# Performance work log

Measured on AMD Instinct MI355X. Metric: run time of the kernel, lower is better.

The kernel has to match this reference:

```python
import jax, jax.numpy as jnp
import numpy as np

B, S, H, L = 64, 512, 768, 9


def setup_inputs() -> dict:
    key = jax.random.key(0)
    ks = jax.random.split(key, 9)
    hidden_states = jax.random.normal(ks[0], (B, S, H), dtype=jnp.float32)
    classifier_w = jax.random.normal(ks[1], (H, L), dtype=jnp.float32) * 0.02
    classifier_b = jax.random.normal(ks[2], (L,), dtype=jnp.float32) * 0.02
    class_weights = jax.random.uniform(ks[3], (L,), dtype=jnp.float32, minval=0.5, maxval=2.0)
    start_transitions = jax.random.normal(ks[4], (L,), dtype=jnp.float32) * 0.1
    end_transitions = jax.random.normal(ks[5], (L,), dtype=jnp.float32) * 0.1
    transitions = jax.random.normal(ks[6], (L, L), dtype=jnp.float32) * 0.1
    labels = jax.random.randint(ks[7], (B, S), 0, L, dtype=jnp.int64)
    special = jax.random.uniform(ks[8], (B, S)) < 0.1
    labels = jnp.where(special, jnp.asarray(-100, labels.dtype), labels)
    # variable-length sequences: attention_mask = 1 for t < length
    lengths = jax.random.randint(jax.random.fold_in(key, 7), (B,), S // 2, S + 1)
    attention_mask = (jnp.arange(S)[None, :] < lengths[:, None]).astype(jnp.int64)
    return dict(hidden_states=hidden_states, classifier_w=classifier_w,
                classifier_b=classifier_b, class_weights=class_weights,
                start_transitions=start_transitions, end_transitions=end_transitions,
                transitions=transitions, labels=labels, attention_mask=attention_mask)


def _crf_nll(emissions, tags, mask, start_transitions, end_transitions, transitions):
    """torchcrf CRF negative log-likelihood, reduction='mean', batch_first.

    emissions: (B, S, L) float; tags: (B, S) int; mask: (B, S) bool (mask[:,0] True).
    """
    Bn, Sn, Ln = emissions.shape
    maskf = mask.astype(emissions.dtype)
    batch_idx = jnp.arange(Bn)

    # ---- numerator: score of the gold tag sequence ----
    emit_tag = jnp.take_along_axis(emissions, tags[:, :, None], axis=2)[:, :, 0]  # (B,S)
    trans_score = transitions[tags[:, :-1], tags[:, 1:]]                            # (B,S-1)
    numerator = (start_transitions[tags[:, 0]] + emit_tag[:, 0]
                 + jnp.sum((trans_score + emit_tag[:, 1:]) * maskf[:, 1:], axis=1))
    last_idx = jnp.sum(mask.astype(jnp.int32), axis=1) - 1                          # (B,)
    numerator = numerator + end_transitions[tags[batch_idx, last_idx]]

    # ---- denominator: forward algorithm (log partition) ----
    score0 = start_transitions[None, :] + emissions[:, 0]                           # (B,L)

    def step(score, inp):
        emit_t, mask_t = inp                                                        # (B,L), (B,)
        # broadcast: (B, from, 1) + (from, to) + (B, 1, to)
        nxt = jax.nn.logsumexp(score[:, :, None] + transitions[None] + emit_t[:, None, :], axis=1)
        score = jnp.where(mask_t[:, None], nxt, score)
        return score, None

    emit_seq = jnp.moveaxis(emissions[:, 1:], 1, 0)   # (S-1, B, L)
    mask_seq = jnp.moveaxis(mask[:, 1:], 1, 0)        # (S-1, B)
    score, _ = jax.lax.scan(step, score0, (emit_seq, mask_seq))
    log_z = jax.nn.logsumexp(score + end_transitions[None, :], axis=1)              # (B,)

    llh = numerator - log_z
    return -jnp.mean(llh)


def reference(hidden_states, classifier_w, classifier_b, class_weights,
              start_transitions, end_transitions, transitions, labels, attention_mask):
    # Linear classifier on BERT output (dropout is identity at eval)
    emissions = jnp.einsum('bsh,hl->bsl', hidden_states, classifier_w) + classifier_b
    emissions = emissions * class_weights[None, None, :]
    # mask/label fixup as in BertCRFModel.forward
    crf_mask = (labels != -100) & (attention_mask == 1)
    crf_mask = crf_mask.at[:, 0].set(True)
    crf_labels = jnp.where(labels == -100, 0, labels)
    return _crf_nll(emissions, crf_labels, crf_mask,
                    start_transitions, end_transitions, transitions)
```

## Files before the change

### kernel.cpp

```cpp
#include <hip/hip_runtime.h>
#include <math.h>

#define Bb 64
#define Ss 512
#define Hh 768
#define Ll 9
#define CCH 32
#define TCH 16
#define NROWS (Bb * Ss)
#define NTILES (NROWS / 16)
#define KSTEPS 24
#define KHALF 12
#define EMIS_SMEM 28672
#define CRF_SMEM  51200

typedef __attribute__((ext_vector_type(8))) short short8;
typedef __attribute__((ext_vector_type(4))) float f32x4;

__device__ __forceinline__ ushort f2bf(float f) {
    unsigned u = __float_as_uint(f);
    return (ushort)((u + 0x7FFFu + ((u >> 16) & 1u)) >> 16);
}
__device__ __forceinline__ float uniform_sgpr(float x) {
    return __int_as_float(__builtin_amdgcn_readfirstlane(__float_as_int(x)));
}

__global__ __launch_bounds__(512, 2) void k_emis(
    const float* __restrict__ hs, const float* __restrict__ W,
    const float* __restrict__ bvec, const float* __restrict__ cw,
    float* __restrict__ emis, float* __restrict__ out)
{
    extern __shared__ char smem[];
    uint4* bpack = (uint4*)smem;
    float* comb  = (float*)(smem + 24576);
    const int tid = threadIdx.x;

    if (blockIdx.x == 0 && tid == 0) out[0] = 0.f;

    const int wid  = tid >> 6;
    const int tl   = wid >> 1;
    const int half = wid & 1;
    const int lane = tid & 63;
    const int col = lane & 15, kg = lane >> 4;
    const int gtile = blockIdx.x * 4 + tl;
    const int row0 = gtile * 16;
    const float* ap = hs + (size_t)(row0 + col) * Hh + kg * 8 + half * (KHALF * 32);

    float4 c0[4], c1[4];
#pragma unroll
    for (int p = 0; p < 4; ++p) {
        c0[p] = *(const float4*)(ap + p * 32);
        c1[p] = *(const float4*)(ap + p * 32 + 4);
    }

    for (int slot = tid; slot < KSTEPS * 64; slot += 512) {
        const int s = slot >> 6, l = slot & 63;
        const int bcol = l & 15, bkg = l >> 4;
        ushort h[8];
#pragma unroll
        for (int j = 0; j < 8; ++j) {
            const int k = s * 32 + bkg * 8 + j;
            h[j] = (bcol < Ll) ? f2bf(W[k * Ll + bcol]) : (ushort)0;
        }
        uint4 u;
        u.x = (unsigned)h[0] | ((unsigned)h[1] << 16);
        u.y = (unsigned)h[2] | ((unsigned)h[3] << 16);
        u.z = (unsigned)h[4] | ((unsigned)h[5] << 16);
        u.w = (unsigned)h[6] | ((unsigned)h[7] << 16);
        bpack[slot] = u;
    }
    __syncthreads();

    f32x4 acc = {0.f, 0.f, 0.f, 0.f};
#pragma unroll
    for (int t = 0; t < KHALF; ++t) {
        const int sl = t & 3;
        const float4 a0 = c0[sl], a1 = c1[sl];
        if (t + 4 < KHALF) {
            c0[sl] = *(const float4*)(ap + (t + 4) * 32);
            c1[sl] = *(const float4*)(ap + (t + 4) * 32 + 4);
        }
        const unsigned x0 = __float_as_uint(a0.x), x1 = __float_as_uint(a0.y);
        const unsigned x2 = __float_as_uint(a0.z), x3 = __float_as_uint(a0.w);
        const unsigned y0 = __float_as_uint(a1.x), y1 = __float_as_uint(a1.y);
        const unsigned y2 = __float_as_uint(a1.z), y3 = __float_as_uint(a1.w);
        uint4 au;
        au.x = (x1 & 0xFFFF0000u) | (x0 >> 16);
        au.y = (x3 & 0xFFFF0000u) | (x2 >> 16);
        au.z = (y1 & 0xFFFF0000u) | (y0 >> 16);
        au.w = (y3 & 0xFFFF0000u) | (y2 >> 16);
        const short8 a = __builtin_bit_cast(short8, au);
        const short8 b = __builtin_bit_cast(short8,
                                            bpack[(half * KHALF + t) * 64 + lane]);
        acc = __builtin_amdgcn_mfma_f32_16x16x32_bf16(a, b, acc, 0, 0, 0);
    }

    if (half == 1) {
#pragma unroll
        for (int j = 0; j < 4; ++j)
            comb[(tl * 4 + j) * 64 + lane] = acc[j];
    }
    __syncthreads();
    if (half == 0) {
#pragma unroll
        for (int j = 0; j < 4; ++j)
            acc[j] += comb[(tl * 4 + j) * 64 + lane];
        if (col < Ll) {
            const float cwv = cw[col], bv = bvec[col];
#pragma unroll
            for (int j = 0; j < 4; ++j)
                emis[(size_t)(row0 + kg * 4 + j) * Ll + col] = (acc[j] + bv) * cwv;
        }
    }
}

__global__ __launch_bounds__(512) void k_crf(
    const float* __restrict__ emis, const int* __restrict__ labels,
    const int* __restrict__ attn, const float* __restrict__ trans,
    const float* __restrict__ startt, const float* __restrict__ endt,
    float* __restrict__ out)
{
    extern __shared__ char smem[];
    int*   mkt_s    = (int*)smem;
    float* emis_s   = (float*)(smem + 2048);
    float* eemis_s  = (float*)(smem + 20480);
    float* trans_s  = (float*)(smem + 38912);
    float* et_s     = (float*)(smem + 39236);
    float* erow_s   = (float*)(smem + 39560);
    float* rowmax_s = (float*)(smem + 49928);
    float* num_s    = (float*)(smem + 51080);

    const int b   = blockIdx.x;
    const int tid = threadIdx.x;

    {
        const int t = tid;
        const int lab = labels[b * Ss + t];
        const int att = attn[b * Ss + t];
        const int tag = (lab == -100) ? 0 : lab;
        const int mk  = ((lab != -100) && (att == 1)) ? 1 : 0;
        mkt_s[t] = tag | (mk << 4);
    }
    {
        const float4* src = (const float4*)(emis + (size_t)b * Ss * Ll);
        float4* dst  = (float4*)emis_s;
        float4* edst = (float4*)eemis_s;
        for (int i = tid; i < (Ss * Ll) / 4; i += 512) {
            const float4 v = src[i];
            dst[i] = v;
            float4 ev;
            ev.x = __expf(v.x); ev.y = __expf(v.y);
            ev.z = __expf(v.z); ev.w = __expf(v.w);
            edst[i] = ev;
        }
    }
    if (tid < Ll * Ll) {
        const float tv = trans[tid];
        trans_s[tid] = tv;
        et_s[tid] = __expf(tv);
    }
    __syncthreads();

    if (tid < CCH * Ll) {
        const int i = tid % Ll;
        const int c = tid / Ll;
        float et[Ll][Ll];
#pragma unroll
        for (int l = 0; l < Ll; ++l)
#pragma unroll
            for (int k = 0; k < Ll; ++k)
                et[l][k] = uniform_sgpr(et_s[l * Ll + k]);

        float u[Ll];
#pragma unroll
        for (int l = 0; l < Ll; ++l) u[l] = (l == i) ? 1.f : 0.f;
        float rlog = 0.f;

        for (int s = (c == 0 ? 1 : 0); s < TCH; ++s) {
            const int t = c * TCH + s;
            const int mv = mkt_s[t];
            if (mv >> 4) {
                const float* ee = eemis_s + t * Ll;
                float nu[Ll];
#pragma unroll
                for (int k = 0; k < Ll; ++k) {
                    float sacc = 0.f;
#pragma unroll
                    for (int l = 0; l < Ll; ++l) sacc = fmaf(u[l], et[l][k], sacc);
                    nu[k] = sacc * ee[k];
                }
#pragma unroll
                for (int l = 0; l < Ll; ++l) u[l] = nu[l];
            }
            if ((s & 3) == 3) {
                float mx = u[0];
#pragma unroll
                for (int l = 1; l < Ll; ++l) mx = fmaxf(mx, u[l]);
                rlog += __logf(mx);
                const float r = 1.f / mx;
#pragma unroll
                for (int l = 0; l < Ll; ++l) u[l] *= r;
            }
        }
        float mx = u[0];
#pragma unroll
        for (int l = 1; l < Ll; ++l) mx = fmaxf(mx, u[l]);
        rowmax_s[c * Ll + i] = rlog + __logf(mx);
        const float r = 1.f / mx;
#pragma unroll
        for (int l = 0; l < Ll; ++l)
            erow_s[(c * Ll + i) * Ll + l] = u[l] * r;
    }

    if (tid >= 448) {
        const int lane = tid - 448;
        float psum = 0.f;
        int pcnt = 0;
        for (int t = lane; t < Ss; t += 64) {
            const int mv  = mkt_s[t];
            const int tag = mv & 15;
            const bool mk = (mv >> 4) || (t == 0);
            if (t >= 1 && (mv >> 4)) {
                const int tagp = mkt_s[t - 1] & 15;
                psum += trans_s[tagp * Ll + tag] + emis_s[t * Ll + tag];
            }
            pcnt += mk ? 1 : 0;
        }
#pragma unroll
        for (int off = 32; off; off >>= 1) {
            psum += __shfl_xor(psum, off);
            pcnt += __shfl_xor(pcnt, off);
        }
        if (lane == 0) {
            const int tag0 = mkt_s[0] & 15;
            const int tagL = mkt_s[pcnt - 1] & 15;
            num_s[0] = startt[tag0] + emis_s[tag0] + psum + endt[tagL];
        }
    }
    __syncthreads();

    if (tid < Ll) {
        const int lane = tid;
        float sc[Ll];
#pragma unroll
        for (int l = 0; l < Ll; ++l) sc[l] = startt[l] + emis_s[l];
        for (int c = 0; c < CCH; ++c) {
            float u[Ll];
#pragma unroll
            for (int l = 0; l < Ll; ++l) u[l] = sc[l] + rowmax_s[c * Ll + l];
            float M = u[0];
#pragma unroll
            for (int l = 1; l < Ll; ++l) M = fmaxf(M, u[l]);
            float sacc = 0.f;
#pragma unroll
            for (int l = 0; l < Ll; ++l)
                sacc = fmaf(__expf(u[l] - M), erow_s[(c * Ll + l) * Ll + lane], sacc);
            const float ns = M + __logf(sacc);
#pragma unroll
            for (int l = 0; l < Ll; ++l) sc[l] = __shfl(ns, l);
        }
        float M2 = sc[0] + endt[0];
#pragma unroll
        for (int l = 1; l < Ll; ++l) M2 = fmaxf(M2, sc[l] + endt[l]);
        float s2 = 0.f;
#pragma unroll
        for (int l = 0; l < Ll; ++l) s2 += __expf(sc[l] + endt[l] - M2);
        if (lane == 0) {
            const float logz = M2 + __logf(s2);
            atomicAdd(out, -(num_s[0] - logz) * (1.f / Bb));
        }
    }
}

extern "C" void kernel_launch(void* const* d_in, const int* in_sizes, int n_in,
                              void* d_out, int out_size, void* d_ws, size_t ws_size,
                              hipStream_t stream)
{
    const float* hs     = (const float*)d_in[0];
    const float* W      = (const float*)d_in[1];
    const float* bvec   = (const float*)d_in[2];
    const float* cw     = (const float*)d_in[3];
    const float* startt = (const float*)d_in[4];
    const float* endt   = (const float*)d_in[5];
    const float* trans  = (const float*)d_in[6];
    const int*   labels = (const int*)d_in[7];
    const int*   attn   = (const int*)d_in[8];
    float* out  = (float*)d_out;
    float* emis = (float*)d_ws;

    hipLaunchKernelGGL(k_emis, dim3(NTILES / 4), dim3(512), EMIS_SMEM, stream,
                       hs, W, bvec, cw, emis, out);
    hipLaunchKernelGGL(k_crf, dim3(Bb), dim3(512), CRF_SMEM, stream,
                       emis, labels, attn, trans, startt, endt, out);
}
```

Before: 45.78 us.

## Store exponentiated emissions padded and stream them directly into CRF registers

The emission kernel now writes exp(emission) into a row-padded buffer with stride 12, so the CRF kernel no longer stages raw and exponentiated emissions in shared memory. Each chunk thread loads its per-step values straight from global memory with double-buffered vector loads, and the block shrinks to 384 threads with far less shared memory. The numerator and the initial scores recover log-emissions through __logf, which adds some rounding error and extra transcendental work. The padded layout also increases workspace writes.

```diff
diff --git a/kernel.cpp b/kernel.cpp
--- a/kernel.cpp
+++ b/kernel.cpp
@@ -11,8 +11,9 @@
 #define NTILES (NROWS / 16)
 #define KSTEPS 24
 #define KHALF 12
+#define EST 12
 #define EMIS_SMEM 28672
-#define CRF_SMEM  51200
+#define CRF_SMEM  14336
 
 typedef __attribute__((ext_vector_type(8))) short short8;
 typedef __attribute__((ext_vector_type(4))) float f32x4;
@@ -28,7 +29,7 @@
 __global__ __launch_bounds__(512, 2) void k_emis(
     const float* __restrict__ hs, const float* __restrict__ W,
     const float* __restrict__ bvec, const float* __restrict__ cw,
-    float* __restrict__ emis, float* __restrict__ out)
+    float* __restrict__ ee2, float* __restrict__ out)
 {
     extern __shared__ char smem[];
     uint4* bpack = (uint4*)smem;
@@ -109,51 +110,36 @@
             const float cwv = cw[col], bv = bvec[col];
 #pragma unroll
             for (int j = 0; j < 4; ++j)
-                emis[(size_t)(row0 + kg * 4 + j) * Ll + col] = (acc[j] + bv) * cwv;
-        }
-    }
-}
-
-__global__ __launch_bounds__(512) void k_crf(
-    const float* __restrict__ emis, const int* __restrict__ labels,
+                ee2[(size_t)(row0 + kg * 4 + j) * EST + col] =
+                    __expf((acc[j] + bv) * cwv);
+        }
+    }
+}
+
+__global__ __launch_bounds__(384) void k_crf(
+    const float* __restrict__ ee2, const int* __restrict__ labels,
     const int* __restrict__ attn, const float* __restrict__ trans,
     const float* __restrict__ startt, const float* __restrict__ endt,
     float* __restrict__ out)
 {
     extern __shared__ char smem[];
     int*   mkt_s    = (int*)smem;
-    float* emis_s   = (float*)(smem + 2048);
-    float* eemis_s  = (float*)(smem + 20480);
-    float* trans_s  = (float*)(smem + 38912);
-    float* et_s     = (float*)(smem + 39236);
-    float* erow_s   = (float*)(smem + 39560);
-    float* rowmax_s = (float*)(smem + 49928);
-    float* num_s    = (float*)(smem + 51080);
+    float* trans_s  = (float*)(smem + 2048);
+    float* et_s     = (float*)(smem + 2372);
+    float* erow_s   = (float*)(smem + 2696);
+    float* rowmax_s = (float*)(smem + 13064);
+    float* num_s    = (float*)(smem + 14216);
 
     const int b   = blockIdx.x;
     const int tid = threadIdx.x;
 
-    {
-        const int t = tid;
+    for (int t = tid; t < Ss; t += 384) {
         const int lab = labels[b * Ss + t];
         const int att = attn[b * Ss + t];
         const int tag = (lab == -100) ? 0 : lab;
         const int mk  = ((lab != -100) && (att == 1)) ? 1 : 0;
         mkt_s[t] = tag | (mk << 4);
     }
-    {
-        const float4* src = (const float4*)(emis + (size_t)b * Ss * Ll);
-        float4* dst  = (float4*)emis_s;
-        float4* edst = (float4*)eemis_s;
-        for (int i = tid; i < (Ss * Ll) / 4; i += 512) {
-            const float4 v = src[i];
-            dst[i] = v;
-            float4 ev;
-            ev.x = __expf(v.x); ev.y = __expf(v.y);
-            ev.z = __expf(v.z); ev.w = __expf(v.w);
-            edst[i] = ev;
-        }
-    }
     if (tid < Ll * Ll) {
         const float tv = trans[tid];
         trans_s[tid] = tv;
@@ -171,23 +157,40 @@
             for (int k = 0; k < Ll; ++k)
                 et[l][k] = uniform_sgpr(et_s[l * Ll + k]);
 
+        const float* ep = ee2 + (size_t)(b * Ss + c * TCH) * EST;
+        float4 p0[2], p1[2]; float p2[2];
+        p0[0] = *(const float4*)ep;
+        p1[0] = *(const float4*)(ep + 4);
+        p2[0] = ep[8];
+
         float u[Ll];
 #pragma unroll
         for (int l = 0; l < Ll; ++l) u[l] = (l == i) ? 1.f : 0.f;
         float rlog = 0.f;
 
-        for (int s = (c == 0 ? 1 : 0); s < TCH; ++s) {
+#pragma unroll
+        for (int s = 0; s < TCH; ++s) {
+            const int cur = s & 1;
+            if (s + 1 < TCH) {
+                const float* np = ep + (s + 1) * EST;
+                p0[cur ^ 1] = *(const float4*)np;
+                p1[cur ^ 1] = *(const float4*)(np + 4);
+                p2[cur ^ 1] = np[8];
+            }
             const int t = c * TCH + s;
             const int mv = mkt_s[t];
-            if (mv >> 4) {
-                const float* ee = eemis_s + t * Ll;
+            if ((c != 0 || s > 0) && (mv >> 4)) {
+                float e[Ll];
+                e[0] = p0[cur].x; e[1] = p0[cur].y; e[2] = p0[cur].z; e[3] = p0[cur].w;
+                e[4] = p1[cur].x; e[5] = p1[cur].y; e[6] = p1[cur].z; e[7] = p1[cur].w;
+                e[8] = p2[cur];
                 float nu[Ll];
 #pragma unroll
                 for (int k = 0; k < Ll; ++k) {
                     float sacc = 0.f;
 #pragma unroll
                     for (int l = 0; l < Ll; ++l) sacc = fmaf(u[l], et[l][k], sacc);
-                    nu[k] = sacc * ee[k];
+                    nu[k] = sacc * e[k];
                 }
 #pragma unroll
                 for (int l = 0; l < Ll; ++l) u[l] = nu[l];
@@ -212,8 +215,8 @@
             erow_s[(c * Ll + i) * Ll + l] = u[l] * r;
     }
 
-    if (tid >= 448) {
-        const int lane = tid - 448;
+    if (tid >= 320) {
+        const int lane = tid - 320;
         float psum = 0.f;
         int pcnt = 0;
         for (int t = lane; t < Ss; t += 64) {
@@ -222,7 +225,8 @@
             const bool mk = (mv >> 4) || (t == 0);
             if (t >= 1 && (mv >> 4)) {
                 const int tagp = mkt_s[t - 1] & 15;
-                psum += trans_s[tagp * Ll + tag] + emis_s[t * Ll + tag];
+                psum += trans_s[tagp * Ll + tag] +
+                        __logf(ee2[(size_t)(b * Ss + t) * EST + tag]);
             }
             pcnt += mk ? 1 : 0;
         }
@@ -234,7 +238,8 @@
         if (lane == 0) {
             const int tag0 = mkt_s[0] & 15;
             const int tagL = mkt_s[pcnt - 1] & 15;
-            num_s[0] = startt[tag0] + emis_s[tag0] + psum + endt[tagL];
+            num_s[0] = startt[tag0] + __logf(ee2[(size_t)(b * Ss) * EST + tag0])
+                       + psum + endt[tagL];
         }
     }
     __syncthreads();
@@ -243,7 +248,8 @@
         const int lane = tid;
         float sc[Ll];
 #pragma unroll
-        for (int l = 0; l < Ll; ++l) sc[l] = startt[l] + emis_s[l];
+        for (int l = 0; l < Ll; ++l)
+            sc[l] = startt[l] + __logf(ee2[(size_t)(b * Ss) * EST + l]);
         for (int c = 0; c < CCH; ++c) {
             float u[Ll];
 #pragma unroll
@@ -285,11 +291,11 @@
     const float* trans  = (const float*)d_in[6];
     const int*   labels = (const int*)d_in[7];
     const int*   attn   = (const int*)d_in[8];
-    float* out  = (float*)d_out;
-    float* emis = (float*)d_ws;
+    float* out = (float*)d_out;
+    float* ee2 = (float*)d_ws;
 
     hipLaunchKernelGGL(k_emis, dim3(NTILES / 4), dim3(512), EMIS_SMEM, stream,
-                       hs, W, bvec, cw, emis, out);
-    hipLaunchKernelGGL(k_crf, dim3(Bb), dim3(512), CRF_SMEM, stream,
-                       emis, labels, attn, trans, startt, endt, out);
-}
+                       hs, W, bvec, cw, ee2, out);
+    hipLaunchKernelGGL(k_crf, dim3(Bb), dim3(384), CRF_SMEM, stream,
+                       ee2, labels, attn, trans, startt, endt, out);
+}
```

After: 44.35 us. 3.1% less time.
